# Kernel optimization log

Hardware: AMD Instinct MI355X
Metric: run time of the kernel (lower is better)

The kernel has to match this reference:

```python
import jax, jax.numpy as jnp
import numpy as np

N, DIM, HEADS, DHEAD = 4096, 1024, 16, 64
INNER = HEADS * DHEAD


def setup_inputs() -> dict:
    key = jax.random.key(0)
    ks = jax.random.split(key, 6)
    s_in = 1.0 / np.sqrt(DIM)
    s_inner = 1.0 / np.sqrt(INNER)
    return {
        "x": jax.random.normal(ks[0], (N, DIM), dtype=jnp.float32),
        # weights stored as (in, out) so y = x @ W
        "Wq": jax.random.uniform(ks[1], (DIM, INNER), jnp.float32, -s_in, s_in),
        "Wk": jax.random.uniform(ks[2], (DIM, INNER), jnp.float32, -s_in, s_in),
        "Wv": jax.random.uniform(ks[3], (DIM, INNER), jnp.float32, -s_in, s_in),
        "Wo": jax.random.uniform(ks[4], (INNER, DIM), jnp.float32, -s_inner, s_inner),
        "bo": jax.random.uniform(ks[5], (DIM,), jnp.float32, -s_inner, s_inner),
    }


def reference(x, Wq, Wk, Wv, Wo, bo):
    scale = DHEAD ** -0.5
    # [n, h, d] -> [h, n, d]
    q = (x @ Wq).reshape(N, HEADS, DHEAD).transpose(1, 0, 2)
    k = (x @ Wk).reshape(N, HEADS, DHEAD).transpose(1, 0, 2)
    v = (x @ Wv).reshape(N, HEADS, DHEAD).transpose(1, 0, 2)
    dots = jnp.einsum("hnd,hmd->hnm", q, k) * scale  # [h, n, n]
    attn = jax.nn.softmax(dots, axis=-1)
    out = jnp.einsum("hnm,hmd->hnd", attn, v)  # [h, n, d]
    out = out.transpose(1, 0, 2).reshape(N, INNER)
    return out @ Wo + bo
```

## Files before the change

kernel.cpp:

```cpp
#include <hip/hip_runtime.h>
#include <cstdint>
#include <cstddef>

typedef _Float16 f16;
typedef _Float16 f16x8 __attribute__((ext_vector_type(8)));
typedef _Float16 f16x4 __attribute__((ext_vector_type(4)));
typedef __fp16 fp16x2 __attribute__((ext_vector_type(2)));
typedef float floatx4 __attribute__((ext_vector_type(4)));
typedef float floatx16 __attribute__((ext_vector_type(16)));

constexpr int SEQ = 4096;
constexpr int DIM = 1024;
constexpr int NHEAD = 16;
constexpr int DH = 64;

#define QSCALE 0.18033688011112042f

__device__ __forceinline__ void async16(void* lds, const void* g) {
  __builtin_amdgcn_global_load_lds(
      (__attribute__((address_space(1))) void*)g,
      (__attribute__((address_space(3))) void*)lds, 16, 0, 0);
}

__device__ __forceinline__ uint32_t pk2(float a, float b) {
  union { fp16x2 h; uint32_t u; } c;
  c.h = __builtin_amdgcn_cvt_pkrtz(a, b);
  return c.u;
}

__device__ __forceinline__ float dot2acc(uint32_t packed, float acc) {
#if __has_builtin(__builtin_amdgcn_fdot2)
  union { uint32_t u; fp16x2 h; } c; c.u = packed;
  fp16x2 one2; one2.x = (__fp16)1.0f; one2.y = (__fp16)1.0f;
  return __builtin_amdgcn_fdot2(c.h, one2, acc, false);
#else
  union { uint32_t u; fp16x2 h; } c; c.u = packed;
  return acc + (float)c.h.x + (float)c.h.y;
#endif
}


__global__ void cvt_x(const float* __restrict__ x, f16* __restrict__ xh) {
  int i = (blockIdx.x * 256 + threadIdx.x) * 4;
  float4 v = *(const float4*)(x + i);
  f16x4 o;
  o.x = (f16)v.x; o.y = (f16)v.y; o.z = (f16)v.z; o.w = (f16)v.w;
  *(f16x4*)(xh + i) = o;
}

__global__ void transpose_cvt(const float* __restrict__ w0, const float* __restrict__ w1,
                              const float* __restrict__ w2, const float* __restrict__ w3,
                              f16* __restrict__ o0, f16* __restrict__ o1,
                              f16* __restrict__ o2, f16* __restrict__ o3) {
  __shared__ float tile[32][33];
  int z = blockIdx.z;
  const float* W = (z == 0) ? w0 : (z == 1) ? w1 : (z == 2) ? w2 : w3;
  f16* O = (z == 0) ? o0 : (z == 1) ? o1 : (z == 2) ? o2 : o3;
  int tx = threadIdx.x, ty = threadIdx.y;
  int xc = blockIdx.x * 32 + tx;
  for (int i = ty; i < 32; i += 8)
    tile[i][tx] = W[(size_t)(blockIdx.y * 32 + i) * DIM + xc];
  __syncthreads();
  int xo = blockIdx.y * 32 + tx;
  for (int i = ty; i < 32; i += 8)
    O[(size_t)(blockIdx.x * 32 + i) * DIM + xo] = (f16)tile[tx][i];
}

__global__ __launch_bounds__(256, 2) void gemm_qkv(
    const f16* __restrict__ xh, const f16* __restrict__ wqt,
    const f16* __restrict__ wkt, const f16* __restrict__ wvt,
    f16* __restrict__ q_ws, f16* __restrict__ k_ws, f16* __restrict__ vt_ws) {
  __shared__ f16 smem[24576];
  const int tid = threadIdx.x;
  const int lane = tid & 63, l16 = lane & 15, quad = lane >> 4;
  const int w = tid >> 6, wr = w >> 1, wc = w & 1;
  const int m0 = blockIdx.x * 128, n0 = blockIdx.y * 256;
  const int z = blockIdx.z;
  const f16* Bt = (z == 0) ? wqt : (z == 1) ? wkt : wvt;

  floatx4 acc[4][8];
#pragma unroll
  for (int mt = 0; mt < 4; ++mt)
#pragma unroll
    for (int nt = 0; nt < 8; ++nt) acc[mt][nt] = (floatx4){0.f, 0.f, 0.f, 0.f};

#define QKV_STAGE(t_, buf_)                                                    \
  {                                                                            \
    int k0_ = (t_) * 32;                                                       \
    _Pragma("unroll")                                                          \
    for (int rnd = 0; rnd < 2; ++rnd) {                                        \
      int e = (rnd * 256 + tid) * 8;                                           \
      int cb = e >> 10, r = (e >> 3) & 127;                                    \
      async16((buf_) + e, xh + (size_t)(m0 + r) * DIM + k0_ + cb * 8);         \
    }                                                                          \
    _Pragma("unroll")                                                          \
    for (int rnd = 0; rnd < 4; ++rnd) {                                        \
      int e = (rnd * 256 + tid) * 8;                                           \
      int cb = e >> 11, r = (e >> 3) & 255;                                    \
      async16((buf_) + 4096 + e, Bt + (size_t)(n0 + r) * DIM + k0_ + cb * 8);  \
    }                                                                          \
  }

  QKV_STAGE(0, smem);
  for (int t = 0; t < 32; ++t) {
    f16* cur = smem + (t & 1) * 12288;
    if (t + 1 < 32) {
      QKV_STAGE(t + 1, smem + ((t + 1) & 1) * 12288);
      asm volatile("s_waitcnt vmcnt(6)" ::: "memory");
    } else {
      asm volatile("s_waitcnt vmcnt(0)" ::: "memory");
    }
    __builtin_amdgcn_s_barrier();
    asm volatile("" ::: "memory");
    const f16* a_lds = cur;
    const f16* b_lds = cur + 4096;
    f16x8 af[4], bq[8];
#pragma unroll
    for (int mt = 0; mt < 4; ++mt)
      af[mt] = *(const f16x8*)(a_lds + quad * 1024 + (wr * 64 + mt * 16 + l16) * 8);
#pragma unroll
    for (int nt = 0; nt < 8; ++nt)
      bq[nt] = *(const f16x8*)(b_lds + quad * 2048 + (wc * 128 + nt * 16 + l16) * 8);
#pragma unroll
    for (int mt = 0; mt < 4; ++mt)
#pragma unroll
      for (int nt = 0; nt < 8; ++nt)
        acc[mt][nt] = __builtin_amdgcn_mfma_f32_16x16x32_f16(af[mt], bq[nt], acc[mt][nt], 0, 0, 0);
    asm volatile("" ::: "memory");
    __builtin_amdgcn_s_barrier();
  }
#undef QKV_STAGE

  if (z < 2) {
#pragma unroll
    for (int mt = 0; mt < 4; ++mt)
#pragma unroll
      for (int nt = 0; nt < 8; ++nt)
#pragma unroll
        for (int r = 0; r < 4; ++r) {
          int m = m0 + wr * 64 + mt * 16 + quad * 4 + r;
          int c = n0 + wc * 128 + nt * 16 + l16;
          float v = acc[mt][nt][r];
          if (z == 0)
            q_ws[(size_t)((c >> 6) * SEQ + m) * DH + (c & 63)] = (f16)(v * QSCALE);
          else
            k_ws[(size_t)((c >> 6) * SEQ + m) * DH + (c & 63)] = (f16)v;
        }
  } else {
#pragma unroll
    for (int ch = 0; ch < 2; ++ch) {
      if (wc == ch) {
#pragma unroll
        for (int mt = 0; mt < 4; ++mt)
#pragma unroll
          for (int nt = 0; nt < 8; ++nt)
#pragma unroll
            for (int r = 0; r < 4; ++r) {
              int cl = nt * 16 + l16;
              int ml = wr * 64 + mt * 16 + quad * 4 + r;
              smem[cl * 132 + ml] = (f16)acc[mt][nt][r];
            }
      }
      __syncthreads();
#pragma unroll
      for (int it = 0; it < 8; ++it) {
        int idx = it * 256 + tid;
        int cl = idx >> 4, mp = (idx & 15) * 8;
        f16x4 lo = *(const f16x4*)(smem + cl * 132 + mp);
        f16x4 hi4 = *(const f16x4*)(smem + cl * 132 + mp + 4);
        f16x8 v8;
#pragma unroll
        for (int j = 0; j < 4; ++j) { v8[j] = lo[j]; v8[4 + j] = hi4[j]; }
        *(f16x8*)(vt_ws + (size_t)(n0 + ch * 128 + cl) * SEQ + m0 + mp) = v8;
      }
      __syncthreads();
    }
  }
}

__global__ __launch_bounds__(256, 4) void attn_kernel(
    const f16* __restrict__ qg, const f16* __restrict__ kg,
    const f16* __restrict__ vtg, f16* __restrict__ po, float* __restrict__ ps) {
  __shared__ f16 smem[16384];

  const int tid = threadIdx.x;
  const int w = tid >> 6, lane = tid & 63, l32 = lane & 31;
  const int hi = lane >> 5;

  const int pid = blockIdx.x + 32 * (blockIdx.y + 16 * blockIdx.z);
  const int vid = (pid & 7) * 128 + (pid >> 3);
  const int qt = vid & 31, h = (vid >> 5) & 15, half = vid >> 9;

  const int q0 = qt * 128 + w * 32;

  f16x8 qf[4];
#pragma unroll
  for (int kf = 0; kf < 4; ++kf)
    qf[kf] = *(const f16x8*)(qg + (size_t)(h * SEQ + q0 + l32) * DH + kf * 16 + hi * 8);

  floatx16 oacc[2];
  oacc[0] = (floatx16)0.f; oacc[1] = (floatx16)0.f;
  float ssa = 0.f, ssb = 0.f;

  const f16* kg_h = kg + (size_t)h * SEQ * DH;
  const f16* vt_h = vtg + (size_t)h * DH * SEQ;
  const int kb0 = half * (SEQ / 128);
  constexpr int NT = SEQ / 128;

  {
    const f16* ks = kg_h + (size_t)(kb0 * 64) * DH;
    const f16* vs = vt_h + kb0 * 64;
#pragma unroll
    for (int rnd = 0; rnd < 2; ++rnd) {
      int e = (rnd * 256 + tid) * 8;
      int cb = e >> 9, r = (e >> 3) & 63;
      async16(smem + e, ks + (size_t)r * DH + cb * 8);
      async16(smem + 4096 + e, vs + (size_t)r * SEQ + cb * 8);
    }
  }

  for (int i = 0; i < NT; ++i) {
    f16* k_lds = smem + (i & 1) * 8192;
    f16* v_lds = k_lds + 4096;
    if (i + 1 < NT) {
      f16* kn = smem + ((i + 1) & 1) * 8192;
      const f16* ks = kg_h + (size_t)((kb0 + i + 1) * 64) * DH;
      const f16* vs = vt_h + (kb0 + i + 1) * 64;
#pragma unroll
      for (int rnd = 0; rnd < 2; ++rnd) {
        int e = (rnd * 256 + tid) * 8;
        int cb = e >> 9, r = (e >> 3) & 63;
        async16(kn + e, ks + (size_t)r * DH + cb * 8);
        async16(kn + 4096 + e, vs + (size_t)r * SEQ + cb * 8);
      }
      asm volatile("s_waitcnt vmcnt(4)" ::: "memory");
    } else {
      asm volatile("s_waitcnt vmcnt(0)" ::: "memory");
    }
    __builtin_amdgcn_s_barrier();
    asm volatile("" ::: "memory");

    floatx16 s0 = (floatx16)0.f, s1 = (floatx16)0.f;
    __builtin_amdgcn_s_setprio(1);
#pragma unroll
    for (int kf = 0; kf < 4; ++kf) {
      const f16* kr = k_lds + (kf * 2 + hi) * 512;
      f16x8 ka = *(const f16x8*)(kr + l32 * 8);
      f16x8 kc = *(const f16x8*)(kr + (32 + l32) * 8);
      s0 = __builtin_amdgcn_mfma_f32_32x32x16_f16(ka, qf[kf], s0, 0, 0, 0);
      s1 = __builtin_amdgcn_mfma_f32_32x32x16_f16(kc, qf[kf], s1, 0, 0, 0);
    }
    __builtin_amdgcn_s_setprio(0);

#pragma unroll
    for (int kb = 0; kb < 2; ++kb) {
      const floatx16 sacc = kb ? s1 : s0;
      f16x8 vf[2][2];
#pragma unroll
      for (int kh = 0; kh < 2; ++kh) {
        int cb = kb * 4 + kh * 2 + hi;
#pragma unroll
        for (int dt = 0; dt < 2; ++dt)
          vf[kh][dt] = *(const f16x8*)(v_lds + cb * 512 + (dt * 32 + l32) * 8);
      }
      float p[16];
#pragma unroll
      for (int r = 0; r < 16; ++r) p[r] = __builtin_amdgcn_exp2f(sacc[r]);
#pragma unroll
      for (int kh = 0; kh < 2; ++kh) {
        uint32_t d0a = pk2(p[8 * kh + 0], p[8 * kh + 1]);
        uint32_t d0b = pk2(p[8 * kh + 2], p[8 * kh + 3]);
        uint32_t d1a = pk2(p[8 * kh + 4], p[8 * kh + 5]);
        uint32_t d1b = pk2(p[8 * kh + 6], p[8 * kh + 7]);
        ssa = dot2acc(d0a, ssa);
        ssa = dot2acc(d0b, ssa);
        ssb = dot2acc(d1a, ssb);
        ssb = dot2acc(d1b, ssb);
        union { uint32_t u[4]; f16x8 v; } bu;
#if __has_builtin(__builtin_amdgcn_permlane32_swap)
        {
          auto sw1 = __builtin_amdgcn_permlane32_swap(d0a, d1a, false, false);
          auto sw2 = __builtin_amdgcn_permlane32_swap(d0b, d1b, false, false);
          bu.u[0] = sw1[0]; bu.u[1] = sw2[0]; bu.u[2] = sw1[1]; bu.u[3] = sw2[1];
        }
#else
        {
          uint32_t ra = (uint32_t)__shfl_xor((int)(hi ? d0a : d1a), 32);
          uint32_t rb = (uint32_t)__shfl_xor((int)(hi ? d0b : d1b), 32);
          bu.u[0] = hi ? ra : d0a;
          bu.u[1] = hi ? rb : d0b;
          bu.u[2] = hi ? d1a : ra;
          bu.u[3] = hi ? d1b : rb;
        }
#endif
        __builtin_amdgcn_s_setprio(1);
#pragma unroll
        for (int dt = 0; dt < 2; ++dt)
          oacc[dt] = __builtin_amdgcn_mfma_f32_32x32x16_f16(vf[kh][dt], bu.v, oacc[dt], 0, 0, 0);
        __builtin_amdgcn_s_setprio(0);
      }
    }
    asm volatile("" ::: "memory");
    __builtin_amdgcn_s_barrier();
    asm volatile("" ::: "memory");
  }

  float ssum = ssa + ssb;
  ssum += __shfl_xor(ssum, 32);
  const int tileid = (half * NHEAD + h) * 32 + qt;
  if (hi == 0) ps[(size_t)tileid * 128 + w * 32 + l32] = ssum;

  f16* pob = po + (size_t)tileid * 8192;
#pragma unroll
  for (int dt = 0; dt < 2; ++dt)
#pragma unroll
    for (int r = 0; r < 16; ++r) {
      int d = dt * 32 + (r & 3) + 8 * (r >> 2) + 4 * hi;
      pob[d * 128 + w * 32 + l32] = (f16)oacc[dt][r];
    }
}

__global__ __launch_bounds__(256, 4) void combine(
    const f16* __restrict__ po, const float* __restrict__ ps, f16* __restrict__ og) {
  __shared__ float inv_s[128];
  __shared__ f16 t[128 * 68];
  const int tid = threadIdx.x;
  const int h = blockIdx.y, qt = blockIdx.x;
  const int t0 = h * 32 + qt, t1 = (NHEAD + h) * 32 + qt;
  if (tid < 128) inv_s[tid] = 1.f / (ps[(size_t)t0 * 128 + tid] + ps[(size_t)t1 * 128 + tid]);
  __syncthreads();
  const f16* b0 = po + (size_t)t0 * 8192;
  const f16* b1 = po + (size_t)t1 * 8192;
#pragma unroll
  for (int it = 0; it < 4; ++it) {
    int e = (it * 256 + tid) * 8;
    int d = e >> 7, q = e & 127;
    f16x8 a = *(const f16x8*)(b0 + e);
    f16x8 b = *(const f16x8*)(b1 + e);
#pragma unroll
    for (int j = 0; j < 8; ++j)
      t[(q + j) * 68 + d] = (f16)(((float)a[j] + (float)b[j]) * inv_s[q + j]);
  }
  __syncthreads();
#pragma unroll
  for (int it = 0; it < 4; ++it) {
    int idx = it * 256 + tid;
    int q = idx >> 3, dcol = (idx & 7) * 8;
    f16x4 lo = *(const f16x4*)(t + q * 68 + dcol);
    f16x4 hi4 = *(const f16x4*)(t + q * 68 + dcol + 4);
    f16x8 v8;
#pragma unroll
    for (int j = 0; j < 4; ++j) { v8[j] = lo[j]; v8[4 + j] = hi4[j]; }
    *(f16x8*)(og + (size_t)(qt * 128 + q) * DIM + h * DH + dcol) = v8;
  }
}

__global__ __launch_bounds__(512, 2) void gemm_o(
    const f16* __restrict__ ab, const f16* __restrict__ wot,
    const float* __restrict__ bo, float* __restrict__ out) {
  __shared__ f16 smem[16384];
  const int tid = threadIdx.x;
  const int lane = tid & 63, l16 = lane & 15, quad = lane >> 4;
  const int w = tid >> 6, wr = w >> 2, wc = w & 3;
  const int m0 = blockIdx.x * 128, n0 = blockIdx.y * 128;

  floatx4 acc[4][2];
#pragma unroll
  for (int mt = 0; mt < 4; ++mt)
#pragma unroll
    for (int nt = 0; nt < 2; ++nt) acc[mt][nt] = (floatx4){0.f, 0.f, 0.f, 0.f};

#define O_STAGE(t_, buf_)                                                      \
  {                                                                            \
    int k0_ = (t_) * 32;                                                       \
    int e = tid * 8;                                                           \
    int cb = e >> 10, r = (e >> 3) & 127;                                      \
    async16((buf_) + e, ab + (size_t)(m0 + r) * DIM + k0_ + cb * 8);           \
    async16((buf_) + 4096 + e, wot + (size_t)(n0 + r) * DIM + k0_ + cb * 8);   \
  }

  O_STAGE(0, smem);
  for (int t = 0; t < 32; ++t) {
    f16* cur = smem + (t & 1) * 8192;
    if (t + 1 < 32) {
      O_STAGE(t + 1, smem + ((t + 1) & 1) * 8192);
      asm volatile("s_waitcnt vmcnt(2)" ::: "memory");
    } else {
      asm volatile("s_waitcnt vmcnt(0)" ::: "memory");
    }
    __builtin_amdgcn_s_barrier();
    asm volatile("" ::: "memory");
    const f16* a_lds = cur;
    const f16* b_lds = cur + 4096;
    f16x8 af[4], bq[2];
#pragma unroll
    for (int mt = 0; mt < 4; ++mt)
      af[mt] = *(const f16x8*)(a_lds + quad * 1024 + (wr * 64 + mt * 16 + l16) * 8);
#pragma unroll
    for (int nt = 0; nt < 2; ++nt)
      bq[nt] = *(const f16x8*)(b_lds + quad * 1024 + (wc * 32 + nt * 16 + l16) * 8);
#pragma unroll
    for (int mt = 0; mt < 4; ++mt)
#pragma unroll
      for (int nt = 0; nt < 2; ++nt)
        acc[mt][nt] = __builtin_amdgcn_mfma_f32_16x16x32_f16(af[mt], bq[nt], acc[mt][nt], 0, 0, 0);
    asm volatile("" ::: "memory");
    __builtin_amdgcn_s_barrier();
  }
#undef O_STAGE

#pragma unroll
  for (int mt = 0; mt < 4; ++mt)
#pragma unroll
    for (int nt = 0; nt < 2; ++nt)
#pragma unroll
      for (int r = 0; r < 4; ++r) {
        int m = m0 + wr * 64 + mt * 16 + quad * 4 + r;
        int c = n0 + wc * 32 + nt * 16 + l16;
        out[(size_t)m * DIM + c] = acc[mt][nt][r] + bo[c];
      }
}


extern "C" void kernel_launch(void* const* d_in, const int* in_sizes, int n_in,
                              void* d_out, int out_size, void* d_ws, size_t ws_size,
                              hipStream_t stream) {
  (void)in_sizes; (void)n_in; (void)out_size; (void)ws_size;
  const float* x  = (const float*)d_in[0];
  const float* Wq = (const float*)d_in[1];
  const float* Wk = (const float*)d_in[2];
  const float* Wv = (const float*)d_in[3];
  const float* Wo = (const float*)d_in[4];
  const float* bo = (const float*)d_in[5];
  float* out = (float*)d_out;
  char* ws = (char*)d_ws;

  f16* xh    = (f16*)(ws);
  f16* wqt   = (f16*)(ws + (8u  << 20));
  f16* wkt   = (f16*)(ws + (10u << 20));
  f16* wvt   = (f16*)(ws + (12u << 20));
  f16* wot   = (f16*)(ws + (14u << 20));
  f16* q_ws  = (f16*)(ws + (16u << 20));
  f16* k_ws  = (f16*)(ws + (24u << 20));
  f16* vt_ws = (f16*)(ws + (32u << 20));
  f16* po    = (f16*)(ws + (40u << 20));
  float* ps  = (float*)(ws + (57u << 20));
  f16* aout  = xh;

  cvt_x<<<dim3(SEQ * DIM / 1024), dim3(256), 0, stream>>>(x, xh);
  transpose_cvt<<<dim3(32, 32, 4), dim3(32, 8), 0, stream>>>(Wq, Wk, Wv, Wo, wqt, wkt, wvt, wot);
  gemm_qkv<<<dim3(32, 4, 3), dim3(256), 0, stream>>>(xh, wqt, wkt, wvt, q_ws, k_ws, vt_ws);
  attn_kernel<<<dim3(SEQ / 128, NHEAD, 2), dim3(256), 0, stream>>>(q_ws, k_ws, vt_ws, po, ps);
  combine<<<dim3(SEQ / 128, NHEAD), dim3(256), 0, stream>>>(po, ps, aout);
  gemm_o<<<dim3(32, 8), dim3(512), 0, stream>>>(aout, wot, bo, out);
}
```

Measured before the change: 246.6 us.

## Drop split-K attention and combine kernel; fuse x conversion into weight prep

Attention no longer splits the key range across two blocks per tile. Each block now walks all 64 key tiles, normalises by its own row sum and writes the transposed output straight to the GEMM input buffer, so the partial-output buffers and the separate combine kernel are gone. The x fp32-to-fp16 conversion is folded into the weight transpose kernel as an extra z-slice, saving one launch. In exchange the attention grid is halved to 512 blocks, which lowers parallelism and occupancy across the CUs.

```diff
diff --git a/kernel.cpp b/kernel.cpp
--- a/kernel.cpp
+++ b/kernel.cpp
@@ -39,21 +39,27 @@
 #endif
 }
 
-
-__global__ void cvt_x(const float* __restrict__ x, f16* __restrict__ xh) {
-  int i = (blockIdx.x * 256 + threadIdx.x) * 4;
-  float4 v = *(const float4*)(x + i);
-  f16x4 o;
-  o.x = (f16)v.x; o.y = (f16)v.y; o.z = (f16)v.z; o.w = (f16)v.w;
-  *(f16x4*)(xh + i) = o;
-}
-
-__global__ void transpose_cvt(const float* __restrict__ w0, const float* __restrict__ w1,
-                              const float* __restrict__ w2, const float* __restrict__ w3,
-                              f16* __restrict__ o0, f16* __restrict__ o1,
-                              f16* __restrict__ o2, f16* __restrict__ o3) {
+__global__ void prep(const float* __restrict__ x, const float* __restrict__ w0,
+                     const float* __restrict__ w1, const float* __restrict__ w2,
+                     const float* __restrict__ w3, f16* __restrict__ xh,
+                     f16* __restrict__ o0, f16* __restrict__ o1,
+                     f16* __restrict__ o2, f16* __restrict__ o3) {
+  int z = blockIdx.z;
+  if (z == 4) {
+    int blk = blockIdx.y * 32 + blockIdx.x;
+    int tid = threadIdx.y * 32 + threadIdx.x;
+    int base = (blk * 256 + tid) * 4;
+#pragma unroll
+    for (int c = 0; c < 4; ++c) {
+      int i = base + c * (SEQ * DIM / 4);
+      float4 v = *(const float4*)(x + i);
+      f16x4 o;
+      o.x = (f16)v.x; o.y = (f16)v.y; o.z = (f16)v.z; o.w = (f16)v.w;
+      *(f16x4*)(xh + i) = o;
+    }
+    return;
+  }
   __shared__ float tile[32][33];
-  int z = blockIdx.z;
   const float* W = (z == 0) ? w0 : (z == 1) ? w1 : (z == 2) ? w2 : w3;
   f16* O = (z == 0) ? o0 : (z == 1) ? o1 : (z == 2) ? o2 : o3;
   int tx = threadIdx.x, ty = threadIdx.y;
@@ -180,16 +186,16 @@
 
 __global__ __launch_bounds__(256, 4) void attn_kernel(
     const f16* __restrict__ qg, const f16* __restrict__ kg,
-    const f16* __restrict__ vtg, f16* __restrict__ po, float* __restrict__ ps) {
+    const f16* __restrict__ vtg, f16* __restrict__ og) {
   __shared__ f16 smem[16384];
 
   const int tid = threadIdx.x;
   const int w = tid >> 6, lane = tid & 63, l32 = lane & 31;
   const int hi = lane >> 5;
 
-  const int pid = blockIdx.x + 32 * (blockIdx.y + 16 * blockIdx.z);
-  const int vid = (pid & 7) * 128 + (pid >> 3);
-  const int qt = vid & 31, h = (vid >> 5) & 15, half = vid >> 9;
+  const int pid = blockIdx.x + 32 * blockIdx.y;
+  const int vid = (pid & 7) * 64 + (pid >> 3);
+  const int qt = vid & 31, h = vid >> 5;
 
   const int q0 = qt * 128 + w * 32;
 
@@ -204,18 +210,15 @@
 
   const f16* kg_h = kg + (size_t)h * SEQ * DH;
   const f16* vt_h = vtg + (size_t)h * DH * SEQ;
-  const int kb0 = half * (SEQ / 128);
-  constexpr int NT = SEQ / 128;
+  constexpr int NT = SEQ / 64;
 
   {
-    const f16* ks = kg_h + (size_t)(kb0 * 64) * DH;
-    const f16* vs = vt_h + kb0 * 64;
 #pragma unroll
     for (int rnd = 0; rnd < 2; ++rnd) {
       int e = (rnd * 256 + tid) * 8;
       int cb = e >> 9, r = (e >> 3) & 63;
-      async16(smem + e, ks + (size_t)r * DH + cb * 8);
-      async16(smem + 4096 + e, vs + (size_t)r * SEQ + cb * 8);
+      async16(smem + e, kg_h + (size_t)r * DH + cb * 8);
+      async16(smem + 4096 + e, vt_h + (size_t)r * SEQ + cb * 8);
     }
   }
 
@@ -224,8 +227,8 @@
     f16* v_lds = k_lds + 4096;
     if (i + 1 < NT) {
       f16* kn = smem + ((i + 1) & 1) * 8192;
-      const f16* ks = kg_h + (size_t)((kb0 + i + 1) * 64) * DH;
-      const f16* vs = vt_h + (kb0 + i + 1) * 64;
+      const f16* ks = kg_h + (size_t)((i + 1) * 64) * DH;
+      const f16* vs = vt_h + (i + 1) * 64;
 #pragma unroll
       for (int rnd = 0; rnd < 2; ++rnd) {
         int e = (rnd * 256 + tid) * 8;
@@ -307,40 +310,20 @@
 
   float ssum = ssa + ssb;
   ssum += __shfl_xor(ssum, 32);
-  const int tileid = (half * NHEAD + h) * 32 + qt;
-  if (hi == 0) ps[(size_t)tileid * 128 + w * 32 + l32] = ssum;
-
-  f16* pob = po + (size_t)tileid * 8192;
+  float rn = 1.f / ssum;
+
+  __syncthreads();
+  f16* t = smem;
+  const int ql = w * 32 + l32;
 #pragma unroll
   for (int dt = 0; dt < 2; ++dt)
 #pragma unroll
-    for (int r = 0; r < 16; ++r) {
-      int d = dt * 32 + (r & 3) + 8 * (r >> 2) + 4 * hi;
-      pob[d * 128 + w * 32 + l32] = (f16)oacc[dt][r];
-    }
-}
-
-__global__ __launch_bounds__(256, 4) void combine(
-    const f16* __restrict__ po, const float* __restrict__ ps, f16* __restrict__ og) {
-  __shared__ float inv_s[128];
-  __shared__ f16 t[128 * 68];
-  const int tid = threadIdx.x;
-  const int h = blockIdx.y, qt = blockIdx.x;
-  const int t0 = h * 32 + qt, t1 = (NHEAD + h) * 32 + qt;
-  if (tid < 128) inv_s[tid] = 1.f / (ps[(size_t)t0 * 128 + tid] + ps[(size_t)t1 * 128 + tid]);
-  __syncthreads();
-  const f16* b0 = po + (size_t)t0 * 8192;
-  const f16* b1 = po + (size_t)t1 * 8192;
-#pragma unroll
-  for (int it = 0; it < 4; ++it) {
-    int e = (it * 256 + tid) * 8;
-    int d = e >> 7, q = e & 127;
-    f16x8 a = *(const f16x8*)(b0 + e);
-    f16x8 b = *(const f16x8*)(b1 + e);
-#pragma unroll
-    for (int j = 0; j < 8; ++j)
-      t[(q + j) * 68 + d] = (f16)(((float)a[j] + (float)b[j]) * inv_s[q + j]);
-  }
+    for (int g = 0; g < 4; ++g) {
+      f16x4 v4;
+#pragma unroll
+      for (int j = 0; j < 4; ++j) v4[j] = (f16)(oacc[dt][g * 4 + j] * rn);
+      *(f16x4*)(t + ql * 68 + dt * 32 + 8 * g + 4 * hi) = v4;
+    }
   __syncthreads();
 #pragma unroll
   for (int it = 0; it < 4; ++it) {
@@ -443,14 +426,10 @@
   f16* q_ws  = (f16*)(ws + (16u << 20));
   f16* k_ws  = (f16*)(ws + (24u << 20));
   f16* vt_ws = (f16*)(ws + (32u << 20));
-  f16* po    = (f16*)(ws + (40u << 20));
-  float* ps  = (float*)(ws + (57u << 20));
   f16* aout  = xh;
 
-  cvt_x<<<dim3(SEQ * DIM / 1024), dim3(256), 0, stream>>>(x, xh);
-  transpose_cvt<<<dim3(32, 32, 4), dim3(32, 8), 0, stream>>>(Wq, Wk, Wv, Wo, wqt, wkt, wvt, wot);
+  prep<<<dim3(32, 32, 5), dim3(32, 8), 0, stream>>>(x, Wq, Wk, Wv, Wo, xh, wqt, wkt, wvt, wot);
   gemm_qkv<<<dim3(32, 4, 3), dim3(256), 0, stream>>>(xh, wqt, wkt, wvt, q_ws, k_ws, vt_ws);
-  attn_kernel<<<dim3(SEQ / 128, NHEAD, 2), dim3(256), 0, stream>>>(q_ws, k_ws, vt_ws, po, ps);
-  combine<<<dim3(SEQ / 128, NHEAD), dim3(256), 0, stream>>>(po, ps, aout);
+  attn_kernel<<<dim3(SEQ / 128, NHEAD), dim3(256), 0, stream>>>(q_ws, k_ws, vt_ws, aout);
   gemm_o<<<dim3(32, 8), dim3(512), 0, stream>>>(aout, wot, bo, out);
 }
```

Measured after the change: 241.6 us. -2.0%, faster.
